# Performance work log

Hardware: AMD Instinct MI355X
Metric: run time of the kernel (lower is better)

The kernel has to match this reference:

```python
import jax, jax.numpy as jnp
import numpy as np

D_MODEL = 512
HEADS = 8
HEAD_DIM = D_MODEL // HEADS
LN_EPS = 1e-5


def _rel_shift(pos_score):
    # pos_score: [B, H, T, P] with P = 2T-1
    B, H, T, P = pos_score.shape
    padded = jnp.pad(pos_score, ((0, 0), (0, 0), (0, 0), (1, 0)))  # [B,H,T,P+1]
    shifted = padded.reshape(B, H, P + 1, T)[:, :, 1:, :].reshape(B, H, T, P)
    return shifted[:, :, :, : P // 2 + 1]  # [B,H,T,T]


def setup_inputs() -> dict:
    key = jax.random.key(0)
    ks = jax.random.split(key, 16)
    B, T = 16, 512
    P = 2 * T - 1
    s = 1.0 / np.sqrt(D_MODEL)
    inp = {
        "x": jax.random.normal(ks[0], (B, T, D_MODEL), jnp.float32),
        "pos_emb": jax.random.normal(ks[1], (B, P, D_MODEL), jnp.float32),
        "ln_g": jnp.ones((D_MODEL,), jnp.float32),
        "ln_b": jnp.zeros((D_MODEL,), jnp.float32),
        "Wq": jax.random.normal(ks[2], (D_MODEL, D_MODEL), jnp.float32) * s,
        "bq": jnp.zeros((D_MODEL,), jnp.float32),
        "Wk": jax.random.normal(ks[3], (D_MODEL, D_MODEL), jnp.float32) * s,
        "bk": jnp.zeros((D_MODEL,), jnp.float32),
        "Wv": jax.random.normal(ks[4], (D_MODEL, D_MODEL), jnp.float32) * s,
        "bv": jnp.zeros((D_MODEL,), jnp.float32),
        "Wp": jax.random.normal(ks[5], (D_MODEL, D_MODEL), jnp.float32) * s,
        "bp": jnp.zeros((D_MODEL,), jnp.float32),
        "content_bias": jax.random.normal(ks[6], (HEADS, HEAD_DIM), jnp.float32) * 0.05,
        "position_bias": jax.random.normal(ks[7], (HEADS, HEAD_DIM), jnp.float32) * 0.05,
        "Wo": jax.random.normal(ks[8], (D_MODEL, D_MODEL), jnp.float32) * s,
        "bo": jnp.zeros((D_MODEL,), jnp.float32),
    }
    return inp


def reference(x, pos_emb, ln_g, ln_b, Wq, bq, Wk, bk, Wv, bv, Wp, bp,
              content_bias, position_bias, Wo, bo):
    B, T, D = x.shape
    H, hd = HEADS, HEAD_DIM

    # LayerNorm over last dim
    mu = jnp.mean(x, axis=-1, keepdims=True)
    var = jnp.var(x, axis=-1, keepdims=True)
    xn = (x - mu) / jnp.sqrt(var + LN_EPS) * ln_g + ln_b

    q = (xn @ Wq.T + bq).reshape(B, T, H, hd)                 # [B,T,H,hd]
    k = (xn @ Wk.T + bk).reshape(B, T, H, hd)                 # [B,T,H,hd]
    v = (xn @ Wv.T + bv).reshape(B, T, H, hd)                 # [B,T,H,hd]
    p = (pos_emb @ Wp.T + bp).reshape(B, -1, H, hd)           # [B,P,H,hd]

    content_score = jnp.einsum('bshd,bthd->bhst', q + content_bias, k)   # [B,H,T,T]
    pos_score = jnp.einsum('bshd,bphd->bhsp', q + position_bias, p)      # [B,H,T,P]
    pos_score = _rel_shift(pos_score)                                    # [B,H,T,T]

    scores = (content_score + pos_score) / jnp.sqrt(jnp.asarray(hd, x.dtype))
    w = jax.nn.softmax(scores, axis=-1)
    ctx = jnp.einsum('bhst,bthd->bshd', w, v).reshape(B, T, D)
    return ctx @ Wo.T + bo
```

## Files before the change

kernel.cpp:

```cpp
#include <hip/hip_runtime.h>
#include <cstdio>
#include <cstdint>


typedef short s16x8 __attribute__((ext_vector_type(8)));
typedef float f32x4 __attribute__((ext_vector_type(4)));
typedef unsigned short u16x4 __attribute__((ext_vector_type(4)));
typedef unsigned short u16x8 __attribute__((ext_vector_type(8)));

#define CSCALE 0.1803368801111204f

#if __has_builtin(__builtin_amdgcn_exp2f)
#define EXP2(x) __builtin_amdgcn_exp2f(x)
#else
#define EXP2(x) exp2f(x)
#endif

__device__ __forceinline__ unsigned short f2bf(float f) {
  unsigned int u = __builtin_bit_cast(unsigned int, f);
  unsigned int r = (u + 0x7FFFu + ((u >> 16) & 1u)) >> 16;
  return (unsigned short)r;
}
__device__ __forceinline__ float bf2f(unsigned short h) {
  unsigned int u = ((unsigned int)h) << 16;
  return __builtin_bit_cast(float, u);
}
__device__ __forceinline__ size_t pk(int row, int col) {
  return (size_t)(row >> 4) * 8192 + (col >> 5) * 512 + ((col >> 3) & 3) * 128 +
         (row & 15) * 8 + (col & 7);
}

__device__ __forceinline__ void gload_lds16(const unsigned short* g,
                                            unsigned short* l) {
  __builtin_amdgcn_global_load_lds(
      (const __attribute__((address_space(1))) unsigned int*)g,
      (__attribute__((address_space(3))) unsigned int*)l, 16, 0, 0);
}

__global__ __launch_bounds__(256) void megaprep(
    const float* __restrict__ x, const float* __restrict__ g,
    const float* __restrict__ bb, unsigned short* __restrict__ xpk,
    const float* __restrict__ pe, unsigned short* __restrict__ pepk,
    const float* __restrict__ Wq, const float* __restrict__ Wk,
    const float* __restrict__ Wp, const float* __restrict__ Wv,
    const float* __restrict__ Wo, const float* __restrict__ bq,
    const float* __restrict__ bk, unsigned short* __restrict__ wqk,
    unsigned short* __restrict__ wpm, unsigned short* __restrict__ wvm,
    unsigned short* __restrict__ wom, float* __restrict__ bqk) {
  const int bid = blockIdx.x, tid = threadIdx.x;
  if (bid < 2048) {
    const int wave = tid >> 6, lane = tid & 63;
    const int row = bid * 4 + wave;
    const int c0 = lane * 8;
    const float* xr = x + (size_t)row * 512 + c0;
    float4 v0 = *(const float4*)xr;
    float4 v1 = *(const float4*)(xr + 4);
    float vv[8] = {v0.x, v0.y, v0.z, v0.w, v1.x, v1.y, v1.z, v1.w};
    float s = 0.f, ss = 0.f;
#pragma unroll
    for (int j = 0; j < 8; ++j) { s += vv[j]; ss += vv[j] * vv[j]; }
#pragma unroll
    for (int d = 1; d < 64; d <<= 1) {
      s += __shfl_xor(s, d, 64);
      ss += __shfl_xor(ss, d, 64);
    }
    const float mu = s * (1.0f / 512.0f);
    const float var = ss * (1.0f / 512.0f) - mu * mu;
    const float rstd = rsqrtf(var + 1e-5f);
    u16x8 o;
#pragma unroll
    for (int j = 0; j < 8; ++j)
      o[j] = f2bf((vv[j] - mu) * rstd * g[c0 + j] + bb[c0 + j]);
    *(u16x8*)(xpk + pk(row, c0)) = o;
  } else if (bid < 6144) {
    int gid = (bid - 2048) * 256 + tid;
    int e = gid * 8;
    int r = e >> 9, c = e & 511;
    int b = r >> 10, u = r & 1023;
    u16x8 o = {0, 0, 0, 0, 0, 0, 0, 0};
    if (u < 1023) {
      const float* src = pe + (size_t)(b * 1023 + u) * 512 + c;
      float4 v0 = *(const float4*)src;
      float4 v1 = *(const float4*)(src + 4);
      o[0] = f2bf(v0.x); o[1] = f2bf(v0.y); o[2] = f2bf(v0.z); o[3] = f2bf(v0.w);
      o[4] = f2bf(v1.x); o[5] = f2bf(v1.y); o[6] = f2bf(v1.z); o[7] = f2bf(v1.w);
    }
    *(u16x8*)(pepk + (size_t)b * 524288 + pk(u, c)) = o;
  } else {
    int gid = (bid - 6144) * 256 + tid;
    int idx = gid * 8;
    int region = idx >> 18, off = idx & 262143;
    const float* src = (region == 0)   ? Wq
                       : (region == 1) ? Wk
                       : (region == 2) ? Wp
                       : (region == 3) ? Wv
                                       : Wo;
    float4 v0 = *(const float4*)(src + off);
    float4 v1 = *(const float4*)(src + off + 4);
    u16x8 o;
    o[0] = f2bf(v0.x); o[1] = f2bf(v0.y); o[2] = f2bf(v0.z); o[3] = f2bf(v0.w);
    o[4] = f2bf(v1.x); o[5] = f2bf(v1.y); o[6] = f2bf(v1.z); o[7] = f2bf(v1.w);
    int n = off >> 9, k = off & 511;
    unsigned short* dst;
    int nrow = n;
    if (region == 0) { dst = wqk; }
    else if (region == 1) { dst = wqk; nrow = n + 512; }
    else if (region == 2) { dst = wpm; }
    else if (region == 3) { dst = wvm; }
    else { dst = wom; }
    *(u16x8*)(dst + pk(nrow, k)) = o;
    if (idx < 1024) {
#pragma unroll
      for (int j = 0; j < 8; j++) {
        int ii = idx + j;
        bqk[ii] = (ii < 512) ? bq[ii] : bk[ii - 512];
      }
    }
  }
}

template <bool SWAP>
__device__ __forceinline__ void strip_gemm(
    const unsigned short* __restrict__ Apk, int astrip4,
    const unsigned short* __restrict__ Bpk, int bstrip4,
    unsigned short* __restrict__ lA, int wave, int lane, f32x4 acc[4][4]) {
  {
    const unsigned short* ga =
        Apk + (size_t)(astrip4 + wave) * 8192 + lane * 8;
    unsigned short* la = lA + wave * 8192;
#pragma unroll
    for (int i = 0; i < 16; ++i) gload_lds16(ga + i * 512, la + i * 512);
  }
  __syncthreads();

  const unsigned short* lrd = lA + lane * 8;
  const unsigned short* gb = Bpk + (size_t)bstrip4 * 8192 + lane * 8;
  s16x8 af[2][4], bf[3][4];
#pragma unroll
  for (int mt = 0; mt < 4; ++mt) af[0][mt] = *(const s16x8*)(lrd + mt * 8192);
#pragma unroll
  for (int nt = 0; nt < 4; ++nt) {
    bf[0][nt] = *(const s16x8*)(gb + (size_t)nt * 8192);
    bf[1][nt] = *(const s16x8*)(gb + (size_t)nt * 8192 + 512);
  }
#pragma unroll
  for (int kc = 0; kc < 16; ++kc) {
    if (kc < 14) {
#pragma unroll
      for (int nt = 0; nt < 4; ++nt)
        bf[(kc + 2) % 3][nt] =
            *(const s16x8*)(gb + (size_t)nt * 8192 + (kc + 2) * 512);
    }
    if (kc < 15) {
#pragma unroll
      for (int mt = 0; mt < 4; ++mt)
        af[(kc + 1) & 1][mt] =
            *(const s16x8*)(lrd + mt * 8192 + (kc + 1) * 512);
    }
#pragma unroll
    for (int mt = 0; mt < 4; ++mt)
#pragma unroll
      for (int nt = 0; nt < 4; ++nt)
        acc[mt][nt] =
            SWAP ? __builtin_amdgcn_mfma_f32_16x16x32_bf16(
                       bf[kc % 3][nt], af[kc & 1][mt], acc[mt][nt], 0, 0, 0)
                 : __builtin_amdgcn_mfma_f32_16x16x32_bf16(
                       af[kc & 1][mt], bf[kc % 3][nt], acc[mt][nt], 0, 0, 0);
  }
}

__global__ __launch_bounds__(256) void proj_all(
    const unsigned short* __restrict__ xpk, const unsigned short* __restrict__ pepk,
    const unsigned short* __restrict__ wqk, const unsigned short* __restrict__ wpm,
    const unsigned short* __restrict__ wvm, const float* __restrict__ bqk,
    const float* __restrict__ bp, const float* __restrict__ bv,
    const float* __restrict__ cbv, const float* __restrict__ pbv,
    unsigned short* __restrict__ qc, unsigned short* __restrict__ qp,
    unsigned short* __restrict__ kb, unsigned short* __restrict__ pbuf,
    unsigned short* __restrict__ vth) {
  __shared__ __align__(16) unsigned short lA[32768];
  const int tid = threadIdx.x, lane = tid & 63, wave = tid >> 6;
  const int bid = blockIdx.x;
  const int fr = lane & 15, hi2 = lane >> 4;
  f32x4 fz = {0.f, 0.f, 0.f, 0.f};
  f32x4 acc[4][4];
#pragma unroll
  for (int i = 0; i < 4; i++)
#pragma unroll
    for (int j = 0; j < 4; j++) acc[i][j] = fz;

  if (bid < 512) {
    int strip = bid >> 2, cg = bid & 3;
    int m0 = strip * 64, n0 = cg * 256 + wave * 64;
    strip_gemm<true>(xpk, strip * 4, wqk, n0 >> 4, lA, wave, lane, acc);
#pragma unroll
    for (int nt = 0; nt < 4; ++nt) {
      int colb = n0 + nt * 16 + hi2 * 4;
      float4 b4 = *(const float4*)(bqk + colb);
      float bvv[4] = {b4.x, b4.y, b4.z, b4.w};
      if (colb < 512) {
        int h = colb >> 6, cc = colb & 63;
        float4 c4 = *(const float4*)(cbv + colb);
        float4 p4 = *(const float4*)(pbv + colb);
        float cvv[4] = {c4.x, c4.y, c4.z, c4.w};
        float pvv[4] = {p4.x, p4.y, p4.z, p4.w};
        size_t cpart = (size_t)(cc >> 5) * 512 + ((cc & 31) >> 3) * 128 +
                       (cc & 7) + (size_t)h * 32768;
#pragma unroll
        for (int mt = 0; mt < 4; ++mt) {
          int row = m0 + mt * 16 + fr;
          int b = row >> 9, s16i = (row & 511) >> 4;
          size_t idx = ((size_t)b * 8 * 32 + s16i) * 1024 + cpart + fr * 8;
          u16x4 oc, op;
#pragma unroll
          for (int r = 0; r < 4; ++r) {
            float val = acc[mt][nt][r] + bvv[r];
            oc[r] = f2bf((val + cvv[r]) * CSCALE);
            op[r] = f2bf((val + pvv[r]) * CSCALE);
          }
          *(u16x4*)(qc + idx) = oc;
          *(u16x4*)(qp + idx) = op;
        }
      } else {
        int c2 = colb - 512, h = c2 >> 6, cc = c2 & 63;
        size_t cpart = (size_t)(cc >> 5) * 512 + ((cc & 31) >> 3) * 128 +
                       (cc & 7) + (size_t)h * 32768;
#pragma unroll
        for (int mt = 0; mt < 4; ++mt) {
          int row = m0 + mt * 16 + fr;
          int b = row >> 9, s16i = (row & 511) >> 4;
          size_t idx = ((size_t)b * 8 * 32 + s16i) * 1024 + cpart + fr * 8;
          u16x4 ok;
#pragma unroll
          for (int r = 0; r < 4; ++r) ok[r] = f2bf(acc[mt][nt][r] + bvv[r]);
          *(u16x4*)(kb + idx) = ok;
        }
      }
    }
  } else if (bid < 1024) {
    int pid = bid - 512;
    int b = pid >> 5, rem = pid & 31;
    int strip16 = rem >> 1, cg = rem & 1;
    int u0 = strip16 * 64, n0 = cg * 256 + wave * 64;
    strip_gemm<true>(pepk + (size_t)b * 524288, strip16 * 4, wpm, n0 >> 4, lA,
                     wave, lane, acc);
#pragma unroll
    for (int nt = 0; nt < 4; ++nt) {
      int colb = n0 + nt * 16 + hi2 * 4;
      float4 b4 = *(const float4*)(bp + colb);
      float bvv[4] = {b4.x, b4.y, b4.z, b4.w};
      int h = colb >> 6, cc = colb & 63;
      size_t cbase = (size_t)(b * 8 + h) * 65536 + (cc >> 5) * 512 +
                     ((cc & 31) >> 3) * 128 + (cc & 7);
#pragma unroll
      for (int mt = 0; mt < 4; ++mt) {
        int u = u0 + mt * 16 + fr;
        size_t idx = cbase + (size_t)(u >> 4) * 1024 + (u & 15) * 8;
        u16x4 o;
        if (u >= 1023) {
          o[0] = 0; o[1] = 0; o[2] = 0; o[3] = 0;
        } else {
#pragma unroll
          for (int r = 0; r < 4; ++r) o[r] = f2bf(acc[mt][nt][r] + bvv[r]);
        }
        *(u16x4*)(pbuf + idx) = o;
      }
    }
  } else {
    int vid = bid - 1024;
    int strip = vid >> 1, cg = vid & 1;
    int m0 = strip * 64, n0 = cg * 256 + wave * 64;
    strip_gemm<false>(xpk, strip * 4, wvm, n0 >> 4, lA, wave, lane, acc);
#pragma unroll
    for (int nt = 0; nt < 4; ++nt) {
      int col = n0 + nt * 16 + fr;
      float bval = bv[col];
      int h = col >> 6, d = col & 63;
#pragma unroll
      for (int mt = 0; mt < 4; ++mt) {
        int rowb = m0 + mt * 16 + hi2 * 4;
        int b = rowb >> 9, t = rowb & 511;
        size_t idx = ((size_t)((b * 8 + h) * 4 + (d >> 4)) * 16 + (t >> 5)) * 512 +
                     ((t & 31) >> 3) * 128 + (d & 15) * 8 + (t & 7);
        u16x4 hv;
#pragma unroll
        for (int r = 0; r < 4; ++r) hv[r] = f2bf(acc[mt][nt][r] + bval);
        *(u16x4*)(vth + idx) = hv;
      }
    }
  }
}

__global__ __launch_bounds__(256) void out_gemm(
    const unsigned short* __restrict__ ctxpk, const unsigned short* __restrict__ wom,
    const float* __restrict__ bo, float* __restrict__ out) {
  __shared__ __align__(16) unsigned short lA[32768];
  const int tid = threadIdx.x, lane = tid & 63, wave = tid >> 6;
  const int bid = blockIdx.x;
  const int fr = lane & 15, hi2 = lane >> 4;
  int strip = bid >> 1, cg = bid & 1;
  int m0 = strip * 64, n0 = cg * 256 + wave * 64;
  f32x4 fz = {0.f, 0.f, 0.f, 0.f};
  f32x4 acc[4][4];
#pragma unroll
  for (int i = 0; i < 4; i++)
#pragma unroll
    for (int j = 0; j < 4; j++) acc[i][j] = fz;
  strip_gemm<true>(ctxpk, strip * 4, wom, n0 >> 4, lA, wave, lane, acc);
#pragma unroll
  for (int nt = 0; nt < 4; ++nt) {
    int colb = n0 + nt * 16 + hi2 * 4;
    float4 b4 = *(const float4*)(bo + colb);
#pragma unroll
    for (int mt = 0; mt < 4; ++mt) {
      int row = m0 + mt * 16 + fr;
      float4 o;
      o.x = acc[mt][nt][0] + b4.x;
      o.y = acc[mt][nt][1] + b4.y;
      o.z = acc[mt][nt][2] + b4.z;
      o.w = acc[mt][nt][3] + b4.w;
      *(float4*)(out + (size_t)row * 512 + colb) = o;
    }
  }
}

__global__ __launch_bounds__(256) void flash_attn(
    const unsigned short* __restrict__ qc, const unsigned short* __restrict__ qp,
    const unsigned short* __restrict__ kb, const unsigned short* __restrict__ pm,
    const unsigned short* __restrict__ vth, unsigned short* __restrict__ ctxpk) {
  const int id = blockIdx.x;
  const int bh = id & 127, b = bh >> 3, h = bh & 7;
  const int s_blk = id >> 7;
  const int tid = threadIdx.x, wave = tid >> 6, lane = tid & 63;
  const int fr = lane & 15, hi2 = lane >> 4, fc = hi2 * 8;
  const int s0w = s_blk * 64 + wave * 16;
  const int crow = hi2 * 4;

  __shared__ __align__(16) unsigned short Ph_s[4][16][40];
  unsigned short(*Phw)[40] = Ph_s[wave];

  int srcl[4];
#pragma unroll
  for (int r = 0; r < 4; ++r) srcl[r] = (hi2 << 4) | ((fr - (crow + r) - 1) & 15);

  const size_t qtb = ((size_t)(b * 8 + h) * 32 + (s0w >> 4)) * 1024 + lane * 8;
  s16x8 aqc0 = *(const s16x8*)(qc + qtb);
  s16x8 aqc1 = *(const s16x8*)(qc + qtb + 512);
  s16x8 aqp0 = *(const s16x8*)(qp + qtb);
  s16x8 aqp1 = *(const s16x8*)(qp + qtb + 512);

  const unsigned short* kpk = kb + (size_t)(b * 8 + h) * 32 * 1024 + lane * 8;
  const unsigned short* ppk = pm + (size_t)(b * 8 + h) * 64 * 1024 + lane * 8;
  const unsigned short* vhk = vth + (size_t)(b * 8 + h) * 64 * 512 + lane * 8;

  f32x4 fz = {0.f, 0.f, 0.f, 0.f};
  f32x4 Oacc[4] = {fz, fz, fz, fz};
  float lsum[4] = {0.f, 0.f, 0.f, 0.f};

  s16x8 kfA[4], pfA[6], vfA[4], kfB[4], pfB[6], vfB[4];

#define LOADF(step, kf, pf, vf)                                              \
  {                                                                          \
    const int t0_ = (step) * 32;                                             \
    const int u0w_ = t0_ - s0w + 496;                                        \
    const int kt_ = t0_ >> 4, ut_ = u0w_ >> 4, vt_ = t0_ >> 5;               \
    _Pragma("unroll") for (int nt = 0; nt < 2; ++nt) {                       \
      const unsigned short* kr = kpk + (size_t)(kt_ + nt) * 1024;            \
      kf[2 * nt] = *(const s16x8*)kr;                                        \
      kf[2 * nt + 1] = *(const s16x8*)(kr + 512);                            \
    }                                                                        \
    _Pragma("unroll") for (int nt = 0; nt < 3; ++nt) {                       \
      const unsigned short* pr = ppk + (size_t)(ut_ + nt) * 1024;            \
      pf[2 * nt] = *(const s16x8*)pr;                                        \
      pf[2 * nt + 1] = *(const s16x8*)(pr + 512);                            \
    }                                                                        \
    _Pragma("unroll") for (int nt = 0; nt < 4; ++nt)                         \
        vf[nt] = *(const s16x8*)(vhk + (size_t)(nt * 16 + vt_) * 512);       \
  }

#define STEPF(kf, pf, vf)                                                    \
  {                                                                          \
    f32x4 sc[2] = {fz, fz};                                                  \
    _Pragma("unroll") for (int nt = 0; nt < 2; ++nt) {                       \
      sc[nt] = __builtin_amdgcn_mfma_f32_16x16x32_bf16(aqc0, kf[2 * nt],     \
                                                       sc[nt], 0, 0, 0);     \
      sc[nt] = __builtin_amdgcn_mfma_f32_16x16x32_bf16(aqc1, kf[2 * nt + 1], \
                                                       sc[nt], 0, 0, 0);     \
    }                                                                        \
    f32x4 sp[3];                                                             \
    _Pragma("unroll") for (int nt = 0; nt < 3; ++nt) {                       \
      f32x4 t = fz;                                                          \
      t = __builtin_amdgcn_mfma_f32_16x16x32_bf16(aqp0, pf[2 * nt], t, 0, 0, 0); \
      t = __builtin_amdgcn_mfma_f32_16x16x32_bf16(aqp1, pf[2 * nt + 1], t, 0, 0, 0); \
      sp[nt] = t;                                                            \
    }                                                                        \
    float sj[3][4];                                                          \
    _Pragma("unroll") for (int j = 0; j < 3; ++j)                            \
        _Pragma("unroll") for (int r = 0; r < 4; ++r)                        \
        sj[j][r] = __shfl(sp[j][r], srcl[r], 64);                            \
    _Pragma("unroll") for (int nt = 0; nt < 2; ++nt) {                       \
      int tc = nt * 16 + fr;                                                 \
      _Pragma("unroll") for (int r = 0; r < 4; ++r) {                        \
        float pos = (fr <= crow + r) ? sj[nt][r] : sj[nt + 1][r];            \
        float e = EXP2(sc[nt][r] + pos);                                     \
        lsum[r] += e;                                                        \
        Phw[crow + r][tc] = f2bf(e);                                         \
      }                                                                      \
    }                                                                        \
    s16x8 ah = *(const s16x8*)&Phw[fr][fc];                                  \
    _Pragma("unroll") for (int nt = 0; nt < 4; ++nt)                         \
        Oacc[nt] = __builtin_amdgcn_mfma_f32_16x16x32_bf16(ah, vf[nt],       \
                                                           Oacc[nt], 0, 0, 0); \
  }

  LOADF(0, kfA, pfA, vfA);
  for (int s2 = 0; s2 < 8; ++s2) {
    LOADF(2 * s2 + 1, kfB, pfB, vfB);
    STEPF(kfA, pfA, vfA);
    if (s2 < 7) LOADF(2 * s2 + 2, kfA, pfA, vfA);
    STEPF(kfB, pfB, vfB);
  }
#undef LOADF
#undef STEPF

#pragma unroll
  for (int d = 1; d < 16; d <<= 1)
#pragma unroll
    for (int r = 0; r < 4; ++r) lsum[r] += __shfl_xor(lsum[r], d, 64);
#pragma unroll
  for (int nt = 0; nt < 4; ++nt)
#pragma unroll
    for (int r = 0; r < 4; ++r) {
      float o = Oacc[nt][r] / lsum[r];
      int row = b * 512 + s0w + crow + r;
      int col = h * 64 + nt * 16 + fr;
      ctxpk[pk(row, col)] = f2bf(o);
    }
}

extern "C" void kernel_launch(void* const* d_in, const int* in_sizes, int n_in,
                              void* d_out, int out_size, void* d_ws,
                              size_t ws_size, hipStream_t stream) {
  const float* x = (const float*)d_in[0];
  const float* pe = (const float*)d_in[1];
  const float* ln_g = (const float*)d_in[2];
  const float* ln_b = (const float*)d_in[3];
  const float* Wq = (const float*)d_in[4];
  const float* bq = (const float*)d_in[5];
  const float* Wk = (const float*)d_in[6];
  const float* bk = (const float*)d_in[7];
  const float* Wv = (const float*)d_in[8];
  const float* bv = (const float*)d_in[9];
  const float* Wp = (const float*)d_in[10];
  const float* bp = (const float*)d_in[11];
  const float* cb = (const float*)d_in[12];
  const float* pb = (const float*)d_in[13];
  const float* Wo = (const float*)d_in[14];
  const float* bo = (const float*)d_in[15];
  float* out = (float*)d_out;

  char* ws = (char*)d_ws;
  size_t off = 0;
  auto alloc = [&](size_t bytes) -> char* {
    char* ptr = ws + off;
    off = (off + bytes + 255) & ~(size_t)255;
    return ptr;
  };
  unsigned short* xpk = (unsigned short*)alloc((size_t)8192 * 512 * 2);
  unsigned short* ctxpk = xpk;
  unsigned short* pepk = (unsigned short*)alloc((size_t)16384 * 512 * 2);
  unsigned short* vt_hi = (unsigned short*)alloc((size_t)8192 * 512 * 2);
  unsigned short* wqk = (unsigned short*)alloc((size_t)1024 * 512 * 2);
  unsigned short* wpm = (unsigned short*)alloc((size_t)512 * 512 * 2);
  unsigned short* wvm = (unsigned short*)alloc((size_t)512 * 512 * 2);
  unsigned short* wom = (unsigned short*)alloc((size_t)512 * 512 * 2);
  float* bqk = (float*)alloc(1024 * 4);
  unsigned short* qc = (unsigned short*)alloc((size_t)8192 * 512 * 2);
  unsigned short* qp = (unsigned short*)alloc((size_t)8192 * 512 * 2);
  unsigned short* kbuf = (unsigned short*)alloc((size_t)8192 * 512 * 2);
  unsigned short* pbuf = (unsigned short*)alloc((size_t)16384 * 512 * 2);

  if (ws_size < off) {
    fprintf(stderr, "kernel_launch: ws too small (need %zu, have %zu)\n", off,
            ws_size);
    return;
  }

  megaprep<<<6784, 256, 0, stream>>>(x, ln_g, ln_b, xpk, pe, pepk, Wq, Wk, Wp,
                                     Wv, Wo, bq, bk, wqk, wpm, wvm, wom, bqk);
  proj_all<<<1280, 256, 0, stream>>>(xpk, pepk, wqk, wpm, wvm, bqk, bp, bv,
                                     cb, pb, qc, qp, kbuf, pbuf, vt_hi);
  flash_attn<<<1024, 256, 0, stream>>>(qc, qp, kbuf, pbuf, vt_hi, ctxpk);
  out_gemm<<<256, 256, 0, stream>>>(ctxpk, wom, bo, out);
}
```

Before: 214.8 us.

## Double per-wave GEMM tile width, swizzle block order, add MFMA priority hints

The projection and output GEMMs now give each wave 128 output columns instead of 64, using two accumulator sets, so each block reuses its LDS-staged A strip across twice as many columns. This halves the grid sizes (640 and 128 blocks). A block-index swizzle interleaves the Q/K, positional and V regions across the grid. In the attention kernel, s_setprio raises wave priority around the MFMA sections. The costs are much higher register pressure from doubled accumulators and B fragments, with possible spills or lower occupancy, and fewer blocks than CUs for out_gemm.

```diff
diff --git a/kernel.cpp b/kernel.cpp
--- a/kernel.cpp
+++ b/kernel.cpp
@@ -120,10 +120,11 @@
 }
 
 template <bool SWAP>
-__device__ __forceinline__ void strip_gemm(
+__device__ __forceinline__ void strip_gemm2(
     const unsigned short* __restrict__ Apk, int astrip4,
     const unsigned short* __restrict__ Bpk, int bstrip4,
-    unsigned short* __restrict__ lA, int wave, int lane, f32x4 acc[4][4]) {
+    unsigned short* __restrict__ lA, int wave, int lane,
+    f32x4 acc0[4][4], f32x4 acc1[4][4]) {
   {
     const unsigned short* ga =
         Apk + (size_t)(astrip4 + wave) * 8192 + lane * 8;
@@ -134,22 +135,28 @@
   __syncthreads();
 
   const unsigned short* lrd = lA + lane * 8;
-  const unsigned short* gb = Bpk + (size_t)bstrip4 * 8192 + lane * 8;
-  s16x8 af[2][4], bf[3][4];
+  const unsigned short* gb0 = Bpk + (size_t)bstrip4 * 8192 + lane * 8;
+  const unsigned short* gb1 = gb0 + (size_t)4 * 8192;
+  s16x8 af[2][4], bf0[3][4], bf1[3][4];
 #pragma unroll
   for (int mt = 0; mt < 4; ++mt) af[0][mt] = *(const s16x8*)(lrd + mt * 8192);
 #pragma unroll
   for (int nt = 0; nt < 4; ++nt) {
-    bf[0][nt] = *(const s16x8*)(gb + (size_t)nt * 8192);
-    bf[1][nt] = *(const s16x8*)(gb + (size_t)nt * 8192 + 512);
+    bf0[0][nt] = *(const s16x8*)(gb0 + (size_t)nt * 8192);
+    bf0[1][nt] = *(const s16x8*)(gb0 + (size_t)nt * 8192 + 512);
+    bf1[0][nt] = *(const s16x8*)(gb1 + (size_t)nt * 8192);
+    bf1[1][nt] = *(const s16x8*)(gb1 + (size_t)nt * 8192 + 512);
   }
 #pragma unroll
   for (int kc = 0; kc < 16; ++kc) {
     if (kc < 14) {
 #pragma unroll
-      for (int nt = 0; nt < 4; ++nt)
-        bf[(kc + 2) % 3][nt] =
-            *(const s16x8*)(gb + (size_t)nt * 8192 + (kc + 2) * 512);
+      for (int nt = 0; nt < 4; ++nt) {
+        bf0[(kc + 2) % 3][nt] =
+            *(const s16x8*)(gb0 + (size_t)nt * 8192 + (kc + 2) * 512);
+        bf1[(kc + 2) % 3][nt] =
+            *(const s16x8*)(gb1 + (size_t)nt * 8192 + (kc + 2) * 512);
+      }
     }
     if (kc < 15) {
 #pragma unroll
@@ -160,12 +167,19 @@
 #pragma unroll
     for (int mt = 0; mt < 4; ++mt)
 #pragma unroll
-      for (int nt = 0; nt < 4; ++nt)
-        acc[mt][nt] =
-            SWAP ? __builtin_amdgcn_mfma_f32_16x16x32_bf16(
-                       bf[kc % 3][nt], af[kc & 1][mt], acc[mt][nt], 0, 0, 0)
-                 : __builtin_amdgcn_mfma_f32_16x16x32_bf16(
-                       af[kc & 1][mt], bf[kc % 3][nt], acc[mt][nt], 0, 0, 0);
+      for (int nt = 0; nt < 4; ++nt) {
+        if (SWAP) {
+          acc0[mt][nt] = __builtin_amdgcn_mfma_f32_16x16x32_bf16(
+              bf0[kc % 3][nt], af[kc & 1][mt], acc0[mt][nt], 0, 0, 0);
+          acc1[mt][nt] = __builtin_amdgcn_mfma_f32_16x16x32_bf16(
+              bf1[kc % 3][nt], af[kc & 1][mt], acc1[mt][nt], 0, 0, 0);
+        } else {
+          acc0[mt][nt] = __builtin_amdgcn_mfma_f32_16x16x32_bf16(
+              af[kc & 1][mt], bf0[kc % 3][nt], acc0[mt][nt], 0, 0, 0);
+          acc1[mt][nt] = __builtin_amdgcn_mfma_f32_16x16x32_bf16(
+              af[kc & 1][mt], bf1[kc % 3][nt], acc1[mt][nt], 0, 0, 0);
+        }
+      }
   }
 }
 
@@ -180,112 +194,126 @@
     unsigned short* __restrict__ vth) {
   __shared__ __align__(16) unsigned short lA[32768];
   const int tid = threadIdx.x, lane = tid & 63, wave = tid >> 6;
-  const int bid = blockIdx.x;
+  int bid = blockIdx.x;
+  bid = (bid & 7) * 80 + (bid >> 3);
   const int fr = lane & 15, hi2 = lane >> 4;
   f32x4 fz = {0.f, 0.f, 0.f, 0.f};
-  f32x4 acc[4][4];
+  f32x4 acc0[4][4], acc1[4][4];
 #pragma unroll
   for (int i = 0; i < 4; i++)
 #pragma unroll
-    for (int j = 0; j < 4; j++) acc[i][j] = fz;
-
-  if (bid < 512) {
-    int strip = bid >> 2, cg = bid & 3;
-    int m0 = strip * 64, n0 = cg * 256 + wave * 64;
-    strip_gemm<true>(xpk, strip * 4, wqk, n0 >> 4, lA, wave, lane, acc);
-#pragma unroll
-    for (int nt = 0; nt < 4; ++nt) {
-      int colb = n0 + nt * 16 + hi2 * 4;
-      float4 b4 = *(const float4*)(bqk + colb);
-      float bvv[4] = {b4.x, b4.y, b4.z, b4.w};
-      if (colb < 512) {
+    for (int j = 0; j < 4; j++) { acc0[i][j] = fz; acc1[i][j] = fz; }
+
+  if (bid < 256) {
+    int strip = bid >> 1, cg = bid & 1;
+    int m0 = strip * 64, n0w = cg * 512 + wave * 128;
+    strip_gemm2<true>(xpk, strip * 4, wqk, n0w >> 4, lA, wave, lane, acc0,
+                      acc1);
+#pragma unroll
+    for (int half = 0; half < 2; ++half) {
+      f32x4(*acch)[4] = half ? acc1 : acc0;
+#pragma unroll
+      for (int nt = 0; nt < 4; ++nt) {
+        int colb = n0w + half * 64 + nt * 16 + hi2 * 4;
+        float4 b4 = *(const float4*)(bqk + colb);
+        float bvv[4] = {b4.x, b4.y, b4.z, b4.w};
+        if (cg == 0) {
+          int h = colb >> 6, cc = colb & 63;
+          float4 c4 = *(const float4*)(cbv + colb);
+          float4 p4 = *(const float4*)(pbv + colb);
+          float cvv[4] = {c4.x, c4.y, c4.z, c4.w};
+          float pvv[4] = {p4.x, p4.y, p4.z, p4.w};
+          size_t cpart = (size_t)(cc >> 5) * 512 + ((cc & 31) >> 3) * 128 +
+                         (cc & 7) + (size_t)h * 32768;
+#pragma unroll
+          for (int mt = 0; mt < 4; ++mt) {
+            int row = m0 + mt * 16 + fr;
+            int b = row >> 9, s16i = (row & 511) >> 4;
+            size_t idx = ((size_t)b * 8 * 32 + s16i) * 1024 + cpart + fr * 8;
+            u16x4 oc, op;
+#pragma unroll
+            for (int r = 0; r < 4; ++r) {
+              float val = acch[mt][nt][r] + bvv[r];
+              oc[r] = f2bf((val + cvv[r]) * CSCALE);
+              op[r] = f2bf((val + pvv[r]) * CSCALE);
+            }
+            *(u16x4*)(qc + idx) = oc;
+            *(u16x4*)(qp + idx) = op;
+          }
+        } else {
+          int c2 = colb - 512, h = c2 >> 6, cc = c2 & 63;
+          size_t cpart = (size_t)(cc >> 5) * 512 + ((cc & 31) >> 3) * 128 +
+                         (cc & 7) + (size_t)h * 32768;
+#pragma unroll
+          for (int mt = 0; mt < 4; ++mt) {
+            int row = m0 + mt * 16 + fr;
+            int b = row >> 9, s16i = (row & 511) >> 4;
+            size_t idx = ((size_t)b * 8 * 32 + s16i) * 1024 + cpart + fr * 8;
+            u16x4 ok;
+#pragma unroll
+            for (int r = 0; r < 4; ++r) ok[r] = f2bf(acch[mt][nt][r] + bvv[r]);
+            *(u16x4*)(kb + idx) = ok;
+          }
+        }
+      }
+    }
+  } else if (bid < 512) {
+    int pid = bid - 256;
+    int b = pid >> 4, strip16 = pid & 15;
+    int u0 = strip16 * 64, n0w = wave * 128;
+    strip_gemm2<true>(pepk + (size_t)b * 524288, strip16 * 4, wpm, n0w >> 4,
+                      lA, wave, lane, acc0, acc1);
+#pragma unroll
+    for (int half = 0; half < 2; ++half) {
+      f32x4(*acch)[4] = half ? acc1 : acc0;
+#pragma unroll
+      for (int nt = 0; nt < 4; ++nt) {
+        int colb = n0w + half * 64 + nt * 16 + hi2 * 4;
+        float4 b4 = *(const float4*)(bp + colb);
+        float bvv[4] = {b4.x, b4.y, b4.z, b4.w};
         int h = colb >> 6, cc = colb & 63;
-        float4 c4 = *(const float4*)(cbv + colb);
-        float4 p4 = *(const float4*)(pbv + colb);
-        float cvv[4] = {c4.x, c4.y, c4.z, c4.w};
-        float pvv[4] = {p4.x, p4.y, p4.z, p4.w};
-        size_t cpart = (size_t)(cc >> 5) * 512 + ((cc & 31) >> 3) * 128 +
-                       (cc & 7) + (size_t)h * 32768;
+        size_t cbase = (size_t)(b * 8 + h) * 65536 + (cc >> 5) * 512 +
+                       ((cc & 31) >> 3) * 128 + (cc & 7);
 #pragma unroll
         for (int mt = 0; mt < 4; ++mt) {
-          int row = m0 + mt * 16 + fr;
-          int b = row >> 9, s16i = (row & 511) >> 4;
-          size_t idx = ((size_t)b * 8 * 32 + s16i) * 1024 + cpart + fr * 8;
-          u16x4 oc, op;
-#pragma unroll
-          for (int r = 0; r < 4; ++r) {
-            float val = acc[mt][nt][r] + bvv[r];
-            oc[r] = f2bf((val + cvv[r]) * CSCALE);
-            op[r] = f2bf((val + pvv[r]) * CSCALE);
+          int u = u0 + mt * 16 + fr;
+          size_t idx = cbase + (size_t)(u >> 4) * 1024 + (u & 15) * 8;
+          u16x4 o;
+          if (u >= 1023) {
+            o[0] = 0; o[1] = 0; o[2] = 0; o[3] = 0;
+          } else {
+#pragma unroll
+            for (int r = 0; r < 4; ++r) o[r] = f2bf(acch[mt][nt][r] + bvv[r]);
           }
-          *(u16x4*)(qc + idx) = oc;
-          *(u16x4*)(qp + idx) = op;
+          *(u16x4*)(pbuf + idx) = o;
         }
-      } else {
-        int c2 = colb - 512, h = c2 >> 6, cc = c2 & 63;
-        size_t cpart = (size_t)(cc >> 5) * 512 + ((cc & 31) >> 3) * 128 +
-                       (cc & 7) + (size_t)h * 32768;
+      }
+    }
+  } else {
+    int strip = bid - 512;
+    int m0 = strip * 64, n0w = wave * 128;
+    strip_gemm2<false>(xpk, strip * 4, wvm, n0w >> 4, lA, wave, lane, acc0,
+                       acc1);
+#pragma unroll
+    for (int half = 0; half < 2; ++half) {
+      f32x4(*acch)[4] = half ? acc1 : acc0;
+#pragma unroll
+      for (int nt = 0; nt < 4; ++nt) {
+        int col = n0w + half * 64 + nt * 16 + fr;
+        float bval = bv[col];
+        int h = col >> 6, d = col & 63;
 #pragma unroll
         for (int mt = 0; mt < 4; ++mt) {
-          int row = m0 + mt * 16 + fr;
-          int b = row >> 9, s16i = (row & 511) >> 4;
-          size_t idx = ((size_t)b * 8 * 32 + s16i) * 1024 + cpart + fr * 8;
-          u16x4 ok;
-#pragma unroll
-          for (int r = 0; r < 4; ++r) ok[r] = f2bf(acc[mt][nt][r] + bvv[r]);
-          *(u16x4*)(kb + idx) = ok;
+          int rowb = m0 + mt * 16 + hi2 * 4;
+          int b = rowb >> 9, t = rowb & 511;
+          size_t idx =
+              ((size_t)((b * 8 + h) * 4 + (d >> 4)) * 16 + (t >> 5)) * 512 +
+              ((t & 31) >> 3) * 128 + (d & 15) * 8 + (t & 7);
+          u16x4 hv;
+#pragma unroll
+          for (int r = 0; r < 4; ++r) hv[r] = f2bf(acch[mt][nt][r] + bval);
+          *(u16x4*)(vth + idx) = hv;
         }
-      }
-    }
-  } else if (bid < 1024) {
-    int pid = bid - 512;
-    int b = pid >> 5, rem = pid & 31;
-    int strip16 = rem >> 1, cg = rem & 1;
-    int u0 = strip16 * 64, n0 = cg * 256 + wave * 64;
-    strip_gemm<true>(pepk + (size_t)b * 524288, strip16 * 4, wpm, n0 >> 4, lA,
-                     wave, lane, acc);
-#pragma unroll
-    for (int nt = 0; nt < 4; ++nt) {
-      int colb = n0 + nt * 16 + hi2 * 4;
-      float4 b4 = *(const float4*)(bp + colb);
-      float bvv[4] = {b4.x, b4.y, b4.z, b4.w};
-      int h = colb >> 6, cc = colb & 63;
-      size_t cbase = (size_t)(b * 8 + h) * 65536 + (cc >> 5) * 512 +
-                     ((cc & 31) >> 3) * 128 + (cc & 7);
-#pragma unroll
-      for (int mt = 0; mt < 4; ++mt) {
-        int u = u0 + mt * 16 + fr;
-        size_t idx = cbase + (size_t)(u >> 4) * 1024 + (u & 15) * 8;
-        u16x4 o;
-        if (u >= 1023) {
-          o[0] = 0; o[1] = 0; o[2] = 0; o[3] = 0;
-        } else {
-#pragma unroll
-          for (int r = 0; r < 4; ++r) o[r] = f2bf(acc[mt][nt][r] + bvv[r]);
-        }
-        *(u16x4*)(pbuf + idx) = o;
-      }
-    }
-  } else {
-    int vid = bid - 1024;
-    int strip = vid >> 1, cg = vid & 1;
-    int m0 = strip * 64, n0 = cg * 256 + wave * 64;
-    strip_gemm<false>(xpk, strip * 4, wvm, n0 >> 4, lA, wave, lane, acc);
-#pragma unroll
-    for (int nt = 0; nt < 4; ++nt) {
-      int col = n0 + nt * 16 + fr;
-      float bval = bv[col];
-      int h = col >> 6, d = col & 63;
-#pragma unroll
-      for (int mt = 0; mt < 4; ++mt) {
-        int rowb = m0 + mt * 16 + hi2 * 4;
-        int b = rowb >> 9, t = rowb & 511;
-        size_t idx = ((size_t)((b * 8 + h) * 4 + (d >> 4)) * 16 + (t >> 5)) * 512 +
-                     ((t & 31) >> 3) * 128 + (d & 15) * 8 + (t & 7);
-        u16x4 hv;
-#pragma unroll
-        for (int r = 0; r < 4; ++r) hv[r] = f2bf(acc[mt][nt][r] + bval);
-        *(u16x4*)(vth + idx) = hv;
       }
     }
   }
@@ -298,28 +326,31 @@
   const int tid = threadIdx.x, lane = tid & 63, wave = tid >> 6;
   const int bid = blockIdx.x;
   const int fr = lane & 15, hi2 = lane >> 4;
-  int strip = bid >> 1, cg = bid & 1;
-  int m0 = strip * 64, n0 = cg * 256 + wave * 64;
+  int m0 = bid * 64, n0w = wave * 128;
   f32x4 fz = {0.f, 0.f, 0.f, 0.f};
-  f32x4 acc[4][4];
+  f32x4 acc0[4][4], acc1[4][4];
 #pragma unroll
   for (int i = 0; i < 4; i++)
 #pragma unroll
-    for (int j = 0; j < 4; j++) acc[i][j] = fz;
-  strip_gemm<true>(ctxpk, strip * 4, wom, n0 >> 4, lA, wave, lane, acc);
-#pragma unroll
-  for (int nt = 0; nt < 4; ++nt) {
-    int colb = n0 + nt * 16 + hi2 * 4;
-    float4 b4 = *(const float4*)(bo + colb);
-#pragma unroll
-    for (int mt = 0; mt < 4; ++mt) {
-      int row = m0 + mt * 16 + fr;
-      float4 o;
-      o.x = acc[mt][nt][0] + b4.x;
-      o.y = acc[mt][nt][1] + b4.y;
-      o.z = acc[mt][nt][2] + b4.z;
-      o.w = acc[mt][nt][3] + b4.w;
-      *(float4*)(out + (size_t)row * 512 + colb) = o;
+    for (int j = 0; j < 4; j++) { acc0[i][j] = fz; acc1[i][j] = fz; }
+  strip_gemm2<true>(ctxpk, bid * 4, wom, n0w >> 4, lA, wave, lane, acc0, acc1);
+#pragma unroll
+  for (int half = 0; half < 2; ++half) {
+    f32x4(*acch)[4] = half ? acc1 : acc0;
+#pragma unroll
+    for (int nt = 0; nt < 4; ++nt) {
+      int colb = n0w + half * 64 + nt * 16 + hi2 * 4;
+      float4 b4 = *(const float4*)(bo + colb);
+#pragma unroll
+      for (int mt = 0; mt < 4; ++mt) {
+        int row = m0 + mt * 16 + fr;
+        float4 o;
+        o.x = acch[mt][nt][0] + b4.x;
+        o.y = acch[mt][nt][1] + b4.y;
+        o.z = acch[mt][nt][2] + b4.z;
+        o.w = acch[mt][nt][3] + b4.w;
+        *(float4*)(out + (size_t)row * 512 + colb) = o;
+      }
     }
   }
 }
@@ -381,6 +412,7 @@
 #define STEPF(kf, pf, vf)                                                    \
   {                                                                          \
     f32x4 sc[2] = {fz, fz};                                                  \
+    __builtin_amdgcn_s_setprio(1);                                           \
     _Pragma("unroll") for (int nt = 0; nt < 2; ++nt) {                       \
       sc[nt] = __builtin_amdgcn_mfma_f32_16x16x32_bf16(aqc0, kf[2 * nt],     \
                                                        sc[nt], 0, 0, 0);     \
@@ -394,6 +426,7 @@
       t = __builtin_amdgcn_mfma_f32_16x16x32_bf16(aqp1, pf[2 * nt + 1], t, 0, 0, 0); \
       sp[nt] = t;                                                            \
     }                                                                        \
+    __builtin_amdgcn_s_setprio(0);                                           \
     float sj[3][4];                                                          \
     _Pragma("unroll") for (int j = 0; j < 3; ++j)                            \
         _Pragma("unroll") for (int r = 0; r < 4; ++r)                        \
@@ -408,9 +441,11 @@
       }                                                                      \
     }                                                                        \
     s16x8 ah = *(const s16x8*)&Phw[fr][fc];                                  \
+    __builtin_amdgcn_s_setprio(1);                                           \
     _Pragma("unroll") for (int nt = 0; nt < 4; ++nt)                         \
         Oacc[nt] = __builtin_amdgcn_mfma_f32_16x16x32_bf16(ah, vf[nt],       \
                                                            Oacc[nt], 0, 0, 0); \
+    __builtin_amdgcn_s_setprio(0);                                           \
   }
 
   LOADF(0, kfA, pfA, vfA);
@@ -488,8 +523,8 @@
 
   megaprep<<<6784, 256, 0, stream>>>(x, ln_g, ln_b, xpk, pe, pepk, Wq, Wk, Wp,
                                      Wv, Wo, bq, bk, wqk, wpm, wvm, wom, bqk);
-  proj_all<<<1280, 256, 0, stream>>>(xpk, pepk, wqk, wpm, wvm, bqk, bp, bv,
-                                     cb, pb, qc, qp, kbuf, pbuf, vt_hi);
+  proj_all<<<640, 256, 0, stream>>>(xpk, pepk, wqk, wpm, wvm, bqk, bp, bv,
+                                    cb, pb, qc, qp, kbuf, pbuf, vt_hi);
   flash_attn<<<1024, 256, 0, stream>>>(qc, qp, kbuf, pbuf, vt_hi, ctxpk);
-  out_gemm<<<256, 256, 0, stream>>>(ctxpk, wom, bo, out);
-}
+  out_gemm<<<128, 256, 0, stream>>>(ctxpk, wom, bo, out);
+}
```

Measured after the change: 221.8 us. +3.3%, slower.

## Switch projection GEMMs to 128x128 double-buffered LDS tiles and add MFMA priority hints

Applied to the files above, without the earlier changes.

The projection and output GEMMs move from 64-row strips, where B fragments are read directly from global memory, to 128x128 block tiles. Both A and B are staged through double-buffered LDS and shared by a 2x2 wave grid. Block IDs are remapped in proj_all to interleave the three work regions across the grid. The attention kernel wraps its MFMA sections in s_setprio so waves issuing matrix ops get scheduling priority. The goal is more operand reuse and better overlap of loads with compute, at the cost of extra barriers per k-step and a different grid decomposition.

```diff
diff --git a/kernel.cpp b/kernel.cpp
--- a/kernel.cpp
+++ b/kernel.cpp
@@ -120,53 +120,55 @@
 }
 
 template <bool SWAP>
-__device__ __forceinline__ void strip_gemm(
-    const unsigned short* __restrict__ Apk, int astrip4,
-    const unsigned short* __restrict__ Bpk, int bstrip4,
-    unsigned short* __restrict__ lA, int wave, int lane, f32x4 acc[4][4]) {
-  {
-    const unsigned short* ga =
-        Apk + (size_t)(astrip4 + wave) * 8192 + lane * 8;
-    unsigned short* la = lA + wave * 8192;
-#pragma unroll
-    for (int i = 0; i < 16; ++i) gload_lds16(ga + i * 512, la + i * 512);
-  }
+__device__ __forceinline__ void gemm128_db(
+    const unsigned short* __restrict__ Apk, int astrip8,
+    const unsigned short* __restrict__ Bpk, int bstrip8,
+    unsigned short* __restrict__ lA, unsigned short* __restrict__ lB,
+    int wave, int lane, f32x4 acc[4][4]) {
+  const int wr = wave >> 1, wc = wave & 1;
+  const unsigned short* ga =
+      Apk + (size_t)(astrip8 + 2 * wave) * 8192 + lane * 8;
+  const unsigned short* gb =
+      Bpk + (size_t)(bstrip8 + 2 * wave) * 8192 + lane * 8;
+#define STG(ks, buf)                                                         \
+  _Pragma("unroll") for (int s = 0; s < 2; ++s) {                            \
+    _Pragma("unroll") for (int hf = 0; hf < 2; ++hf) {                       \
+      gload_lds16(ga + (size_t)s * 8192 + (ks) * 1024 + hf * 512,            \
+                  lA + (buf) * 8192 + (2 * wave + s) * 1024 + hf * 512);     \
+      gload_lds16(gb + (size_t)s * 8192 + (ks) * 1024 + hf * 512,            \
+                  lB + (buf) * 8192 + (2 * wave + s) * 1024 + hf * 512);     \
+    }                                                                        \
+  }
+  STG(0, 0);
   __syncthreads();
-
-  const unsigned short* lrd = lA + lane * 8;
-  const unsigned short* gb = Bpk + (size_t)bstrip4 * 8192 + lane * 8;
-  s16x8 af[2][4], bf[3][4];
-#pragma unroll
-  for (int mt = 0; mt < 4; ++mt) af[0][mt] = *(const s16x8*)(lrd + mt * 8192);
-#pragma unroll
-  for (int nt = 0; nt < 4; ++nt) {
-    bf[0][nt] = *(const s16x8*)(gb + (size_t)nt * 8192);
-    bf[1][nt] = *(const s16x8*)(gb + (size_t)nt * 8192 + 512);
-  }
-#pragma unroll
-  for (int kc = 0; kc < 16; ++kc) {
-    if (kc < 14) {
+  const unsigned short* lar = lA + (wr * 4) * 1024 + lane * 8;
+  const unsigned short* lbr = lB + (wc * 4) * 1024 + lane * 8;
+#pragma unroll
+  for (int ks = 0; ks < 8; ++ks) {
+    const int cur = ks & 1;
+    if (ks < 7) { STG(ks + 1, cur ^ 1); }
+#pragma unroll
+    for (int kk = 0; kk < 2; ++kk) {
+      s16x8 af[4], bf[4];
+#pragma unroll
+      for (int mt = 0; mt < 4; ++mt)
+        af[mt] = *(const s16x8*)(lar + cur * 8192 + mt * 1024 + kk * 512);
 #pragma unroll
       for (int nt = 0; nt < 4; ++nt)
-        bf[(kc + 2) % 3][nt] =
-            *(const s16x8*)(gb + (size_t)nt * 8192 + (kc + 2) * 512);
-    }
-    if (kc < 15) {
+        bf[nt] = *(const s16x8*)(lbr + cur * 8192 + nt * 1024 + kk * 512);
 #pragma unroll
       for (int mt = 0; mt < 4; ++mt)
-        af[(kc + 1) & 1][mt] =
-            *(const s16x8*)(lrd + mt * 8192 + (kc + 1) * 512);
-    }
-#pragma unroll
-    for (int mt = 0; mt < 4; ++mt)
-#pragma unroll
-      for (int nt = 0; nt < 4; ++nt)
-        acc[mt][nt] =
-            SWAP ? __builtin_amdgcn_mfma_f32_16x16x32_bf16(
-                       bf[kc % 3][nt], af[kc & 1][mt], acc[mt][nt], 0, 0, 0)
-                 : __builtin_amdgcn_mfma_f32_16x16x32_bf16(
-                       af[kc & 1][mt], bf[kc % 3][nt], acc[mt][nt], 0, 0, 0);
-  }
+#pragma unroll
+        for (int nt = 0; nt < 4; ++nt)
+          acc[mt][nt] =
+              SWAP ? __builtin_amdgcn_mfma_f32_16x16x32_bf16(
+                         bf[nt], af[mt], acc[mt][nt], 0, 0, 0)
+                   : __builtin_amdgcn_mfma_f32_16x16x32_bf16(
+                         af[mt], bf[nt], acc[mt][nt], 0, 0, 0);
+    }
+    __syncthreads();
+  }
+#undef STG
 }
 
 __global__ __launch_bounds__(256) void proj_all(
@@ -178,9 +180,12 @@
     unsigned short* __restrict__ qc, unsigned short* __restrict__ qp,
     unsigned short* __restrict__ kb, unsigned short* __restrict__ pbuf,
     unsigned short* __restrict__ vth) {
-  __shared__ __align__(16) unsigned short lA[32768];
+  __shared__ __align__(16) unsigned short lA[16384];
+  __shared__ __align__(16) unsigned short lB[16384];
   const int tid = threadIdx.x, lane = tid & 63, wave = tid >> 6;
-  const int bid = blockIdx.x;
+  int bid = blockIdx.x;
+  bid = (bid & 7) * 160 + (bid >> 3);
+  const int wr = wave >> 1, wc = wave & 1;
   const int fr = lane & 15, hi2 = lane >> 4;
   f32x4 fz = {0.f, 0.f, 0.f, 0.f};
   f32x4 acc[4][4];
@@ -190,9 +195,9 @@
     for (int j = 0; j < 4; j++) acc[i][j] = fz;
 
   if (bid < 512) {
-    int strip = bid >> 2, cg = bid & 3;
-    int m0 = strip * 64, n0 = cg * 256 + wave * 64;
-    strip_gemm<true>(xpk, strip * 4, wqk, n0 >> 4, lA, wave, lane, acc);
+    int m_t = bid >> 3, n_t = bid & 7;
+    gemm128_db<true>(xpk, m_t * 8, wqk, n_t * 8, lA, lB, wave, lane, acc);
+    int m0 = m_t * 128 + wr * 64, n0 = n_t * 128 + wc * 64;
 #pragma unroll
     for (int nt = 0; nt < 4; ++nt) {
       int colb = n0 + nt * 16 + hi2 * 4;
@@ -240,10 +245,10 @@
   } else if (bid < 1024) {
     int pid = bid - 512;
     int b = pid >> 5, rem = pid & 31;
-    int strip16 = rem >> 1, cg = rem & 1;
-    int u0 = strip16 * 64, n0 = cg * 256 + wave * 64;
-    strip_gemm<true>(pepk + (size_t)b * 524288, strip16 * 4, wpm, n0 >> 4, lA,
-                     wave, lane, acc);
+    int m_tb = rem >> 2, n_t = rem & 3;
+    gemm128_db<true>(pepk + (size_t)b * 524288, m_tb * 8, wpm, n_t * 8, lA,
+                     lB, wave, lane, acc);
+    int u0 = m_tb * 128 + wr * 64, n0 = n_t * 128 + wc * 64;
 #pragma unroll
     for (int nt = 0; nt < 4; ++nt) {
       int colb = n0 + nt * 16 + hi2 * 4;
@@ -268,9 +273,9 @@
     }
   } else {
     int vid = bid - 1024;
-    int strip = vid >> 1, cg = vid & 1;
-    int m0 = strip * 64, n0 = cg * 256 + wave * 64;
-    strip_gemm<false>(xpk, strip * 4, wvm, n0 >> 4, lA, wave, lane, acc);
+    int m_t = vid >> 2, n_t = vid & 3;
+    gemm128_db<false>(xpk, m_t * 8, wvm, n_t * 8, lA, lB, wave, lane, acc);
+    int m0 = m_t * 128 + wr * 64, n0 = n_t * 128 + wc * 64;
 #pragma unroll
     for (int nt = 0; nt < 4; ++nt) {
       int col = n0 + nt * 16 + fr;
@@ -280,8 +285,9 @@
       for (int mt = 0; mt < 4; ++mt) {
         int rowb = m0 + mt * 16 + hi2 * 4;
         int b = rowb >> 9, t = rowb & 511;
-        size_t idx = ((size_t)((b * 8 + h) * 4 + (d >> 4)) * 16 + (t >> 5)) * 512 +
-                     ((t & 31) >> 3) * 128 + (d & 15) * 8 + (t & 7);
+        size_t idx =
+            ((size_t)((b * 8 + h) * 4 + (d >> 4)) * 16 + (t >> 5)) * 512 +
+            ((t & 31) >> 3) * 128 + (d & 15) * 8 + (t & 7);
         u16x4 hv;
 #pragma unroll
         for (int r = 0; r < 4; ++r) hv[r] = f2bf(acc[mt][nt][r] + bval);
@@ -294,19 +300,21 @@
 __global__ __launch_bounds__(256) void out_gemm(
     const unsigned short* __restrict__ ctxpk, const unsigned short* __restrict__ wom,
     const float* __restrict__ bo, float* __restrict__ out) {
-  __shared__ __align__(16) unsigned short lA[32768];
+  __shared__ __align__(16) unsigned short lA[16384];
+  __shared__ __align__(16) unsigned short lB[16384];
   const int tid = threadIdx.x, lane = tid & 63, wave = tid >> 6;
   const int bid = blockIdx.x;
+  const int wr = wave >> 1, wc = wave & 1;
   const int fr = lane & 15, hi2 = lane >> 4;
-  int strip = bid >> 1, cg = bid & 1;
-  int m0 = strip * 64, n0 = cg * 256 + wave * 64;
+  int m_t = bid >> 2, n_t = bid & 3;
   f32x4 fz = {0.f, 0.f, 0.f, 0.f};
   f32x4 acc[4][4];
 #pragma unroll
   for (int i = 0; i < 4; i++)
 #pragma unroll
     for (int j = 0; j < 4; j++) acc[i][j] = fz;
-  strip_gemm<true>(ctxpk, strip * 4, wom, n0 >> 4, lA, wave, lane, acc);
+  gemm128_db<true>(ctxpk, m_t * 8, wom, n_t * 8, lA, lB, wave, lane, acc);
+  int m0 = m_t * 128 + wr * 64, n0 = n_t * 128 + wc * 64;
 #pragma unroll
   for (int nt = 0; nt < 4; ++nt) {
     int colb = n0 + nt * 16 + hi2 * 4;
@@ -381,6 +389,7 @@
 #define STEPF(kf, pf, vf)                                                    \
   {                                                                          \
     f32x4 sc[2] = {fz, fz};                                                  \
+    __builtin_amdgcn_s_setprio(1);                                           \
     _Pragma("unroll") for (int nt = 0; nt < 2; ++nt) {                       \
       sc[nt] = __builtin_amdgcn_mfma_f32_16x16x32_bf16(aqc0, kf[2 * nt],     \
                                                        sc[nt], 0, 0, 0);     \
@@ -394,6 +403,7 @@
       t = __builtin_amdgcn_mfma_f32_16x16x32_bf16(aqp1, pf[2 * nt + 1], t, 0, 0, 0); \
       sp[nt] = t;                                                            \
     }                                                                        \
+    __builtin_amdgcn_s_setprio(0);                                           \
     float sj[3][4];                                                          \
     _Pragma("unroll") for (int j = 0; j < 3; ++j)                            \
         _Pragma("unroll") for (int r = 0; r < 4; ++r)                        \
@@ -408,9 +418,11 @@
       }                                                                      \
     }                                                                        \
     s16x8 ah = *(const s16x8*)&Phw[fr][fc];                                  \
+    __builtin_amdgcn_s_setprio(1);                                           \
     _Pragma("unroll") for (int nt = 0; nt < 4; ++nt)                         \
         Oacc[nt] = __builtin_amdgcn_mfma_f32_16x16x32_bf16(ah, vf[nt],       \
                                                            Oacc[nt], 0, 0, 0); \
+    __builtin_amdgcn_s_setprio(0);                                           \
   }
 
   LOADF(0, kfA, pfA, vfA);
```

Result: no change. 215.8 us (+0.5%).
